# Optimization experiments

Measured on AMD Instinct MI355X. Metric: run time of the kernel, lower is better.

## Reference

```python
import jax, jax.numpy as jnp
import numpy as np

HIDDEN = 4096
NUM_HEADS = 32
HEAD_DIM = 128
NUM_KV_HEADS = 8
KV_GROUPS = NUM_HEADS // NUM_KV_HEADS
ROPE_THETA = 10000.0
SEQ = 2048
BATCH = 1
NEG_INF = -1e9


def fake_quant_int8(x):
    """Per-tensor symmetric int8 fake quantization (absmax scale)."""
    scale = jnp.maximum(jnp.max(jnp.abs(x)) / 127.0, 1e-8)
    q = jnp.clip(jnp.round(x / scale), -127.0, 127.0) * scale
    # straight-through estimator (no-op in fwd-only, keeps code shared)
    return x + jax.lax.stop_gradient(q - x)


def rotate_half(x):
    x1, x2 = jnp.split(x, 2, axis=-1)
    return jnp.concatenate([-x2, x1], axis=-1)


def rope_cos_sin(position_ids):
    inv_freq = 1.0 / (ROPE_THETA ** (jnp.arange(0, HEAD_DIM, 2, dtype=jnp.float32) / HEAD_DIM))
    freqs = position_ids.astype(jnp.float32)[..., None] * inv_freq  # [B,S,HD/2]
    emb = jnp.concatenate([freqs, freqs], axis=-1)                  # [B,S,HD]
    return jnp.cos(emb), jnp.sin(emb)


def setup_inputs() -> dict:
    key = jax.random.key(0)
    k1, k2, k3, k4, k5 = jax.random.split(key, 5)
    hidden_states = jax.random.normal(k1, (BATCH, SEQ, HIDDEN), dtype=jnp.float32)
    causal = jnp.tril(jnp.ones((SEQ, SEQ), dtype=bool))
    attention_mask = jnp.where(causal, 0.0, NEG_INF).astype(jnp.float32)[None, None]  # [1,1,S,S]
    position_ids = jnp.arange(SEQ, dtype=jnp.int64 if jax.config.jax_enable_x64 else jnp.int32)[None, :]
    s = 0.02
    wq = jax.random.normal(k2, (NUM_HEADS * HEAD_DIM, HIDDEN), dtype=jnp.float32) * s
    wk = jax.random.normal(k3, (NUM_KV_HEADS * HEAD_DIM, HIDDEN), dtype=jnp.float32) * s
    wv = jax.random.normal(k4, (NUM_KV_HEADS * HEAD_DIM, HIDDEN), dtype=jnp.float32) * s
    wo = jax.random.normal(k5, (HIDDEN, NUM_HEADS * HEAD_DIM), dtype=jnp.float32) * s
    return {"hidden_states": hidden_states, "attention_mask": attention_mask,
            "position_ids": position_ids, "wq": wq, "wk": wk, "wv": wv, "wo": wo}


def reference(hidden_states, attention_mask, position_ids, wq, wk, wv, wo):
    B, S, _ = hidden_states.shape

    def qlinear(x, w):  # quantized linear: fake-quant act and weight, y = x @ w.T
        return fake_quant_int8(x) @ fake_quant_int8(w).T

    q = qlinear(hidden_states, wq).reshape(B, S, NUM_HEADS, HEAD_DIM).transpose(0, 2, 1, 3)
    k = qlinear(hidden_states, wk).reshape(B, S, NUM_KV_HEADS, HEAD_DIM).transpose(0, 2, 1, 3)
    v = qlinear(hidden_states, wv).reshape(B, S, NUM_KV_HEADS, HEAD_DIM).transpose(0, 2, 1, 3)

    cos, sin = rope_cos_sin(position_ids)      # [B,S,HD]
    cos, sin = cos[:, None], sin[:, None]      # [B,1,S,HD]
    q = q * cos + rotate_half(q) * sin
    k = k * cos + rotate_half(k) * sin

    # repeat_kv: GQA -> full heads
    k = jnp.repeat(k, KV_GROUPS, axis=1)
    v = jnp.repeat(v, KV_GROUPS, axis=1)

    # quantized QK^T
    scores = jnp.einsum('bhqd,bhkd->bhqk', fake_quant_int8(q), fake_quant_int8(k))
    scores = scores * (1.0 / np.sqrt(HEAD_DIM).astype(np.float32))
    scores = scores + attention_mask[:, :, :, :S]
    probs = jax.nn.softmax(scores.astype(jnp.float32), axis=-1).astype(q.dtype)
    # attention_dropout = 0.0 -> identity

    # quantized AV
    attn_out = jnp.einsum('bhqk,bhkd->bhqd', fake_quant_int8(probs), fake_quant_int8(v))
    attn_out = attn_out.transpose(0, 2, 1, 3).reshape(B, S, NUM_HEADS * HEAD_DIM)
    return qlinear(attn_out, wo)
```

## Files before the change

kernel.cpp:

```cpp
#include <hip/hip_runtime.h>
#include <stdint.h>

#define SEQ   2048
#define HID   4096
#define NH    32
#define NKV   8
#define KVDIM 1024
#define KVCAT 2048

typedef int v4i __attribute__((ext_vector_type(4)));

#define VMCNT0 asm volatile("s_waitcnt vmcnt(0)" ::: "memory")

__device__ __forceinline__ void gload16(const void* g, void* l) {
    __builtin_amdgcn_global_load_lds(
        (const __attribute__((address_space(1))) void*)(uintptr_t)g,
        (__attribute__((address_space(3))) void*)(uintptr_t)l, 16, 0, 0);
}

__device__ __forceinline__ float slot_scale(const unsigned* slots, int slot) {
    return fmaxf(__uint_as_float(slots[slot << 5]) / 127.0f, 1e-8f);
}

__device__ __forceinline__ int q8v(float x, float s) {
    int v = (int)rintf(x / s);
    return v < -127 ? -127 : (v > 127 ? 127 : v);
}

__device__ __forceinline__ float fexp2(float x) {
    float r; asm("v_exp_f32 %0, %1" : "=v"(r) : "v"(x)); return r;
}

__device__ __forceinline__ float amax4(const float* __restrict__ p, long v) {
    float4 x = *(const float4*)(p + v * 4);
    return fmaxf(fmaxf(fabsf(x.x), fabsf(x.y)), fmaxf(fabsf(x.z), fabsf(x.w)));
}

__device__ __forceinline__ void block_amax_part(float m, float* dst) {
    __shared__ float sm[4];
    int lane = threadIdx.x & 63, w = threadIdx.x >> 6;
    for (int off = 32; off; off >>= 1) m = fmaxf(m, __shfl_xor(m, off, 64));
    if (lane == 0) sm[w] = m;
    __syncthreads();
    if (threadIdx.x == 0)
        *dst = fmaxf(fmaxf(sm[0], sm[1]), fmaxf(sm[2], sm[3]));
    __syncthreads();
}

#define NV0 ((long)SEQ * HID / 4)
#define NV1 ((long)HID * HID / 4)
#define NV2 ((long)KVDIM * HID / 4)
__global__ void k_absmax5(const float* __restrict__ a0, const float* __restrict__ a1,
                          const float* __restrict__ a2, const float* __restrict__ a3,
                          const float* __restrict__ a4, float* __restrict__ part) {
    int b = blockIdx.x;
    const float* p; long n; int lb, nb;
    if (b < 342)       { p = a0; n = NV0; lb = b;        nb = 342; }
    else if (b < 1025) { p = a1; n = NV1; lb = b - 342;  nb = 683; }
    else if (b < 1196) { p = a2; n = NV2; lb = b - 1025; nb = 171; }
    else if (b < 1367) { p = a3; n = NV2; lb = b - 1196; nb = 171; }
    else               { p = a4; n = NV1; lb = b - 1367; nb = 681; }
    long str = (long)nb * 256;
    float mm[8] = {0.f, 0.f, 0.f, 0.f, 0.f, 0.f, 0.f, 0.f};
    long v = (long)lb * 256 + threadIdx.x;
    for (; v + 7 * str < n; v += 8 * str) {
        #pragma unroll
        for (int j = 0; j < 8; j++) mm[j] = fmaxf(mm[j], amax4(p, v + j * str));
    }
    for (; v < n; v += str) mm[0] = fmaxf(mm[0], amax4(p, v));
    float m = fmaxf(fmaxf(fmaxf(mm[0], mm[1]), fmaxf(mm[2], mm[3])),
                    fmaxf(fmaxf(mm[4], mm[5]), fmaxf(mm[6], mm[7])));
    block_amax_part(m, part + blockIdx.x);
}

__global__ void k_reduceA(const float* __restrict__ part, unsigned* slots) {
    __shared__ float sm[4];
    const int lo[5] = {0, 342, 1025, 1196, 1367};
    const int hi[5] = {342, 1025, 1196, 1367, 2048};
    int t = threadIdx.x, lane = t & 63, w = t >> 6;
    for (int s = 0; s < 5; s++) {
        float m = 0.f;
        for (int i = lo[s] + t; i < hi[s]; i += 256) m = fmaxf(m, part[i]);
        for (int off = 32; off; off >>= 1) m = fmaxf(m, __shfl_xor(m, off, 64));
        if (lane == 0) sm[w] = m;
        __syncthreads();
        if (t == 0)
            slots[s << 5] = __float_as_uint(fmaxf(fmaxf(sm[0], sm[1]), fmaxf(sm[2], sm[3])));
        __syncthreads();
    }
}

__global__ void k_reduceB(const float* __restrict__ p1, const float* __restrict__ p2,
                          const float* __restrict__ p3, unsigned* slots) {
    __shared__ float sm[4];
    int t = threadIdx.x, lane = t & 63, w = t >> 6;
    const float* ps[3] = {p1, p2, p3};
    const int cnt[3] = {512, 128, 128};
    const int sl[3] = {5, 6, 7};
    for (int s = 0; s < 3; s++) {
        float m = 0.f;
        for (int i = t; i < cnt[s]; i += 256) m = fmaxf(m, ps[s][i]);
        for (int off = 32; off; off >>= 1) m = fmaxf(m, __shfl_xor(m, off, 64));
        if (lane == 0) sm[w] = m;
        __syncthreads();
        if (t == 0)
            slots[sl[s] << 5] = __float_as_uint(fmaxf(fmaxf(sm[0], sm[1]), fmaxf(sm[2], sm[3])));
        __syncthreads();
    }
}

__device__ __forceinline__ void qstore4(const float* __restrict__ src, long v,
                                        int8_t* __restrict__ dst, float s) {
    float4 x = *(const float4*)(src + v * 4);
    unsigned pa = (unsigned)(uint8_t)(int8_t)q8v(x.x, s)
                | ((unsigned)(uint8_t)(int8_t)q8v(x.y, s) << 8)
                | ((unsigned)(uint8_t)(int8_t)q8v(x.z, s) << 16)
                | ((unsigned)(uint8_t)(int8_t)q8v(x.w, s) << 24);
    *(unsigned*)(dst + v * 4) = pa;
}

__global__ void k_quant4(const float* __restrict__ a0, const float* __restrict__ a1,
                         const float* __restrict__ a2, const float* __restrict__ a3,
                         int8_t* __restrict__ d0, int8_t* __restrict__ d1,
                         int8_t* __restrict__ d2, int8_t* __restrict__ d3,
                         const unsigned* __restrict__ slots) {
    int b = blockIdx.x;
    const float* p; int8_t* d; long n; int slot, lb, nb;
    if (b < 512)       { p = a0; d = d0; n = NV0; slot = 0; lb = b;        nb = 512; }
    else if (b < 1536) { p = a1; d = d1; n = NV1; slot = 1; lb = b - 512;  nb = 1024; }
    else if (b < 1792) { p = a2; d = d2; n = NV2; slot = 2; lb = b - 1536; nb = 256; }
    else               { p = a3; d = d3; n = NV2; slot = 3; lb = b - 1792; nb = 256; }
    float s = slot_scale(slots, slot);
    long str = (long)nb * 256;
    long v = (long)lb * 256 + threadIdx.x;
    for (; v + 3 * str < n; v += 4 * str) {
        #pragma unroll
        for (int j = 0; j < 4; j++) qstore4(p, v + j * str, d, s);
    }
    for (; v < n; v += str) qstore4(p, v, d, s);
}

__global__ void k_quant(const float* __restrict__ x, int8_t* __restrict__ q, long nvec,
                        int rshift, long cmaskv, long ld,
                        const unsigned* __restrict__ slots, int slot) {
    float s = slot_scale(slots, slot);
    long gs = (long)gridDim.x * blockDim.x;
    long v = blockIdx.x * (long)blockDim.x + threadIdx.x;
    for (; v + 3 * gs < nvec; v += 4 * gs) {
        #pragma unroll
        for (int j = 0; j < 4; j++) {
            long vid = v + j * gs;
            long r = vid >> rshift;
            long c = (vid & cmaskv) << 2;
            float4 vv = *(const float4*)(x + r * ld + c);
            unsigned pa = (unsigned)(uint8_t)(int8_t)q8v(vv.x, s)
                        | ((unsigned)(uint8_t)(int8_t)q8v(vv.y, s) << 8)
                        | ((unsigned)(uint8_t)(int8_t)q8v(vv.z, s) << 16)
                        | ((unsigned)(uint8_t)(int8_t)q8v(vv.w, s) << 24);
            *(unsigned*)(q + vid * 4) = pa;
        }
    }
    for (; v < nvec; v += gs) {
        long r = v >> rshift;
        long c = (v & cmaskv) << 2;
        float4 vv = *(const float4*)(x + r * ld + c);
        unsigned pa = (unsigned)(uint8_t)(int8_t)q8v(vv.x, s)
                    | ((unsigned)(uint8_t)(int8_t)q8v(vv.y, s) << 8)
                    | ((unsigned)(uint8_t)(int8_t)q8v(vv.z, s) << 16)
                    | ((unsigned)(uint8_t)(int8_t)q8v(vv.w, s) << 24);
        *(unsigned*)(q + v * 4) = pa;
    }
}

__global__ void k_ropetab(const int* __restrict__ pos, float* __restrict__ ct,
                          float* __restrict__ st) {
    int tid = blockIdx.x * blockDim.x + threadIdx.x;
    if (tid >= SEQ * 64) return;
    int i = tid & 63, s = tid >> 6;
    double inv = 1.0 / pow(10000.0, (double)((float)(2 * i) * (1.0f / 128.0f)));
    float invf = (float)inv;
    float angf = (float)pos[s] * invf;
    double a = (double)angf;
    ct[tid] = (float)cos(a);
    st[tid] = (float)sin(a);
}

__global__ void k_transq(const float* __restrict__ src, long lds_, int8_t* __restrict__ dst,
                         long ldd, const unsigned* __restrict__ slots, int slot) {
    __shared__ float t[32][33];
    float s = slot_scale(slots, slot);
    int bx = blockIdx.x, by = blockIdx.y;
    int tid = threadIdx.x;
    int c = tid & 31, r0 = tid >> 5;
    #pragma unroll
    for (int j = 0; j < 4; j++) {
        int r = r0 + j * 8;
        t[r][c] = src[(long)(by * 32 + r) * lds_ + bx * 32 + c];
    }
    __syncthreads();
    int d = tid >> 3, k4 = (tid & 7) * 4;
    unsigned pa = 0;
    #pragma unroll
    for (int j = 0; j < 4; j++) {
        int iv = q8v(t[k4 + j][d], s);
        pa |= ((unsigned)(uint8_t)(int8_t)iv) << (8 * j);
    }
    *(unsigned*)(dst + (long)(bx * 32 + d) * ldd + by * 32 + k4) = pa;
}

__global__ __launch_bounds__(256) void k_gemm_i8(
    const int8_t* __restrict__ A, const int8_t* __restrict__ B, float* __restrict__ C,
    int M, int N, int K, unsigned* slots,
    int slotA, int slotB, int slotB2, int nsplit,
    float* pQ, float* pK, float* pV, int ropemode,
    const float* __restrict__ ct, const float* __restrict__ st) {
    __shared__ int8_t POOL[65536];
    int8_t (*As)[16384] = (int8_t(*)[16384])POOL;
    int8_t (*Bs)[16384] = (int8_t(*)[16384])(POOL + 32768);
    const v4i vzero = {0, 0, 0, 0};
    int tid = threadIdx.x, lane = tid & 63, wid = tid >> 6;
    int nbx = N >> 7;
    int nwg = gridDim.x, wg = blockIdx.x;
    int cpx = nwg >> 3;
    int swz = (wg & 7) * cpx + (wg >> 3);
    int bm = swz / nbx, bn = swz % nbx;
    long rowA0 = (long)bm * 128, colB0 = (long)bn * 128;
    int wrow = (wid >> 1) * 64, wcol = (wid & 1) * 64;
    int lr = lane >> 3;
    int swc = ((lane & 7) ^ lr) * 16;
    const int8_t* ga = A + (rowA0 + wid * 8 + lr) * (long)K + swc;
    const int8_t* gb = B + (colB0 + wid * 8 + lr) * (long)K + swc;
    v4i acc[4][4];
    #pragma unroll
    for (int m = 0; m < 4; m++)
        #pragma unroll
        for (int n = 0; n < 4; n++) acc[m][n] = vzero;

    auto STAGE = [&](int buf, int kt) {
        #pragma unroll
        for (int i = 0; i < 4; i++) {
            gload16(ga + kt + (long)(i * 32) * K, &As[buf][(wid * 8 + i * 32) * 128]);
            gload16(gb + kt + (long)(i * 32) * K, &Bs[buf][(wid * 8 + i * 32) * 128]);
        }
    };
    auto COMPUTE = [&](int buf) {
        #pragma unroll
        for (int ks = 0; ks < 2; ks++) {
            v4i af[4], bf[4];
            #pragma unroll
            for (int m = 0; m < 4; m++) {
                int row = wrow + m * 16 + (lane & 15);
                af[m] = *(const v4i*)(&As[buf][row * 128 + (((ks * 4 + (lane >> 4)) ^ (row & 7)) * 16)]);
            }
            #pragma unroll
            for (int n = 0; n < 4; n++) {
                int row = wcol + n * 16 + (lane & 15);
                bf[n] = *(const v4i*)(&Bs[buf][row * 128 + (((ks * 4 + (lane >> 4)) ^ (row & 7)) * 16)]);
            }
            #pragma unroll
            for (int m = 0; m < 4; m++)
                #pragma unroll
                for (int n = 0; n < 4; n++)
                    acc[m][n] = __builtin_amdgcn_mfma_i32_16x16x64_i8(af[m], bf[n], acc[m][n], 0, 0, 0);
        }
    };

    STAGE(0, 0);
    VMCNT0;
    __syncthreads();
    int nt = K >> 7, cur = 0;
    for (int t = 0; t < nt - 1; t++) {
        STAGE(cur ^ 1, (t + 1) << 7);
        COMPUTE(cur);
        VMCNT0;
        __syncthreads();
        cur ^= 1;
    }
    COMPUTE(cur);

    float sA = slot_scale(slots, slotA);
    float sB1 = slot_scale(slots, slotB);
    float sB2 = slot_scale(slots, slotB2);
    int qc = lane & 15, rgrp = (lane >> 4) << 2;
    if (ropemode == 1 || (ropemode == 2 && bn < 8)) {
        __syncthreads();
        float* EX = (float*)POOL;
        #pragma unroll
        for (int m = 0; m < 4; m++)
            #pragma unroll
            for (int n = 0; n < 4; n++) {
                int coll = wcol + n * 16 + qc;
                #pragma unroll
                for (int r = 0; r < 4; r++) {
                    int rowl = wrow + m * 16 + rgrp + r;
                    EX[rowl * 128 + (coll ^ ((rowl & 1) << 4))] = sA * sB1 * (float)acc[m][n][r];
                }
            }
        __syncthreads();
        float am = 0.f;
        #pragma unroll
        for (int m = 0; m < 4; m++)
            #pragma unroll
            for (int n = 0; n < 4; n++) {
                int coll = wcol + n * 16 + qc;
                #pragma unroll
                for (int r = 0; r < 4; r++) {
                    int rowl = wrow + m * 16 + rgrp + r;
                    long srow = rowA0 + rowl;
                    float self = EX[rowl * 128 + (coll ^ ((rowl & 1) << 4))];
                    float pv = EX[rowl * 128 + ((coll ^ 64) ^ ((rowl & 1) << 4))];
                    float c = ct[srow * 64 + (coll & 63)];
                    float sn = st[srow * 64 + (coll & 63)];
                    float o = (coll < 64) ? self * c - pv * sn : self * c + pv * sn;
                    am = fmaxf(am, fabsf(o));
                    C[srow * N + colB0 + coll] = o;
                }
            }
        block_amax_part(am, (ropemode == 1) ? pQ + blockIdx.x : pK + bm * 8 + (bn & 7));
    } else if (ropemode == 2) {
        float am = 0.f;
        #pragma unroll
        for (int m = 0; m < 4; m++) {
            long row0 = rowA0 + wrow + m * 16 + rgrp;
            #pragma unroll
            for (int n = 0; n < 4; n++) {
                int col = (int)colB0 + wcol + n * 16 + qc;
                float sc = sA * ((col < nsplit) ? sB1 : sB2);
                float* cp = C + row0 * N + col;
                #pragma unroll
                for (int r = 0; r < 4; r++) {
                    float val = sc * (float)acc[m][n][r];
                    cp[(long)r * N] = val;
                    am = fmaxf(am, fabsf(val));
                }
            }
        }
        block_amax_part(am, pV + bm * 8 + (bn & 7));
    } else {
        #pragma unroll
        for (int m = 0; m < 4; m++) {
            long row0 = rowA0 + wrow + m * 16 + rgrp;
            #pragma unroll
            for (int n = 0; n < 4; n++) {
                int col = (int)colB0 + wcol + n * 16 + qc;
                float sc = sA * ((col < nsplit) ? sB1 : sB2);
                float* cp = C + row0 * N + col;
                #pragma unroll
                for (int r = 0; r < 4; r++) cp[(long)r * N] = sc * (float)acc[m][n][r];
            }
        }
    }
}

__global__ __launch_bounds__(256) void k_attn(
    const int8_t* __restrict__ Qq, const int8_t* __restrict__ Kq, const int8_t* __restrict__ Vtq,
    int* __restrict__ AO, unsigned* slots) {
    __shared__ int8_t Qs[64 * 128];
    __shared__ int8_t Ks[2][64 * 128];
    __shared__ int8_t Vs[2][128 * 64];
    __shared__ int smx[4];
    const v4i vzero = {0, 0, 0, 0};
    const int NEGS = -(1 << 29);
    const float MAGIC = 12582912.0f;
    int tid = threadIdx.x, lane = tid & 63, w = tid >> 6;
    int qlan = lane & 15, g = lane >> 4;
    int idx = blockIdx.x;
    int qb = 31 - (idx >> 5), h = idx & 31, kvh = h >> 2;
    float sq = slot_scale(slots, 5), sk = slot_scale(slots, 6);
    float c2 = sq * sk * 0.08838834764831845f * 1.4426950408889634f;
    int lr8 = lane >> 3;
    int swc = ((lane & 7) ^ lr8) * 16;
    int lr4 = lane >> 2;
    int vswc = ((lane & 3) ^ (lr4 & 3)) * 16;
    const int8_t* kbase = Kq + ((long)(w * 8 + lr8)) * KVDIM + kvh * 128 + swc;
    const int8_t* vbase = Vtq + ((long)kvh * 128 + w * 16 + lr4) * SEQ + vswc;
    auto STAGE_K = [&](int buf, int kt) {
        #pragma unroll
        for (int i = 0; i < 2; i++)
            gload16(kbase + ((long)kt * 64 + i * 32) * KVDIM, &Ks[buf][(w * 8 + i * 32) * 128]);
    };
    auto STAGE_V = [&](int buf, int kt) {
        #pragma unroll
        for (int i = 0; i < 2; i++)
            gload16(vbase + (long)(i * 64) * SEQ + kt * 64, &Vs[buf][(w * 16 + i * 64) * 64]);
    };
    {
        const int8_t* qbase = Qq + ((long)qb * 64 + w * 8 + lr8) * HID + h * 128 + swc;
        #pragma unroll
        for (int i = 0; i < 2; i++)
            gload16(qbase + (long)(i * 32) * HID, &Qs[(w * 8 + i * 32) * 128]);
    }
    STAGE_K(0, 0);
    VMCNT0;
    __syncthreads();
    v4i aq[2];
    #pragma unroll
    for (int ks = 0; ks < 2; ks++) {
        int row = w * 16 + qlan;
        aq[ks] = *(const v4i*)(&Qs[row * 128 + (((ks * 4 + g) ^ (row & 7)) * 16)]);
    }
    int mi = -(1 << 30);
    float l = 0.f;
    int buf = 0;
    for (int kt = 0; kt <= qb; kt++) {
        if (kt < qb) STAGE_K(buf ^ 1, kt + 1);
        v4i sf[4] = {vzero, vzero, vzero, vzero};
        __builtin_amdgcn_s_setprio(1);
        #pragma unroll
        for (int ks = 0; ks < 2; ks++)
            #pragma unroll
            for (int f = 0; f < 4; f++) {
                int row = f * 16 + qlan;
                v4i bk = *(const v4i*)(&Ks[buf][row * 128 + (((ks * 4 + g) ^ (row & 7)) * 16)]);
                sf[f] = __builtin_amdgcn_mfma_i32_16x16x64_i8(bk, aq[ks], sf[f], 0, 0, 0);
            }
        __builtin_amdgcn_s_setprio(0);
        int sv[16];
        if (kt == qb) {
            int qthr = w * 16 + qlan;
            #pragma unroll
            for (int f = 0; f < 4; f++)
                #pragma unroll
                for (int r = 0; r < 4; r++) {
                    int kl = f * 16 + g * 4 + r;
                    sv[f * 4 + r] = (kl > qthr) ? NEGS : sf[f][r];
                }
        } else {
            #pragma unroll
            for (int f = 0; f < 4; f++)
                #pragma unroll
                for (int r = 0; r < 4; r++) sv[f * 4 + r] = sf[f][r];
        }
        int tm = sv[0];
        #pragma unroll
        for (int e = 1; e < 16; e++) tm = tm > sv[e] ? tm : sv[e];
        tm = max(tm, __shfl_xor(tm, 16, 64));
        tm = max(tm, __shfl_xor(tm, 32, 64));
        int mn = tm > mi ? tm : mi;
        float nb = -c2 * (float)mn;
        float esc = fexp2(fmaf((float)mi, c2, nb));
        float es = 0.f;
        #pragma unroll
        for (int e = 0; e < 16; e++) es += fexp2(fmaf((float)sv[e], c2, nb));
        es += __shfl_xor(es, 16, 64);
        es += __shfl_xor(es, 32, 64);
        l = l * esc + es;
        mi = mn;
        VMCNT0;
        __syncthreads();
        buf ^= 1;
    }
    float Bq = fmaf(c2, (float)mi, __log2f(l) - 6.9886846867721655f);
    unsigned* Ps32 = (unsigned*)Qs;
    int pwr = w * 320;
    v4i of[8];
    #pragma unroll
    for (int nf = 0; nf < 8; nf++) of[nf] = vzero;
    STAGE_K(0, 0);
    STAGE_V(0, 0);
    VMCNT0;
    __syncthreads();
    buf = 0;
    for (int kt = 0; kt <= qb; kt++) {
        if (kt < qb) { STAGE_K(buf ^ 1, kt + 1); STAGE_V(buf ^ 1, kt + 1); }
        v4i sf[4] = {vzero, vzero, vzero, vzero};
        __builtin_amdgcn_s_setprio(1);
        #pragma unroll
        for (int ks = 0; ks < 2; ks++)
            #pragma unroll
            for (int f = 0; f < 4; f++) {
                int row = f * 16 + qlan;
                v4i bk = *(const v4i*)(&Ks[buf][row * 128 + (((ks * 4 + g) ^ (row & 7)) * 16)]);
                sf[f] = __builtin_amdgcn_mfma_i32_16x16x64_i8(bk, aq[ks], sf[f], 0, 0, 0);
            }
        __builtin_amdgcn_s_setprio(0);
        if (kt == qb) {
            int qthr = w * 16 + qlan;
            #pragma unroll
            for (int f = 0; f < 4; f++) {
                unsigned pk = 0;
                #pragma unroll
                for (int r = 0; r < 4; r++) {
                    int kl = f * 16 + g * 4 + r;
                    int s = (kl > qthr) ? NEGS : sf[f][r];
                    float t = fexp2(fmaf((float)s, c2, -Bq));
                    unsigned u = __float_as_uint(t + MAGIC) & 127u;
                    pk |= u << (8 * r);
                }
                Ps32[pwr + (4 * f + g) * 20 + qlan] = pk;
            }
        } else {
            #pragma unroll
            for (int f = 0; f < 4; f++) {
                unsigned pk = 0;
                #pragma unroll
                for (int r = 0; r < 4; r++) {
                    float t = fexp2(fmaf((float)sf[f][r], c2, -Bq));
                    unsigned u = __float_as_uint(t + MAGIC) & 127u;
                    pk |= u << (8 * r);
                }
                Ps32[pwr + (4 * f + g) * 20 + qlan] = pk;
            }
        }
        int rb = pwr + 80 * g + qlan;
        v4i ap;
        ap[0] = (int)Ps32[rb];
        ap[1] = (int)Ps32[rb + 20];
        ap[2] = (int)Ps32[rb + 40];
        ap[3] = (int)Ps32[rb + 60];
        __builtin_amdgcn_s_setprio(1);
        #pragma unroll
        for (int nf = 0; nf < 8; nf++) {
            int row = nf * 16 + qlan;
            v4i bv = *(const v4i*)(&Vs[buf][row * 64 + ((g ^ (row & 3)) * 16)]);
            of[nf] = __builtin_amdgcn_mfma_i32_16x16x64_i8(ap, bv, of[nf], 0, 0, 0);
        }
        __builtin_amdgcn_s_setprio(0);
        VMCNT0;
        __syncthreads();
        buf ^= 1;
    }
    int mymax = 0;
    #pragma unroll
    for (int nf = 0; nf < 8; nf++)
        #pragma unroll
        for (int r = 0; r < 4; r++) {
            int val = of[nf][r];
            int av = val < 0 ? -val : val;
            mymax = av > mymax ? av : mymax;
            int qg = qb * 64 + w * 16 + 4 * g + r;
            AO[(long)qg * HID + h * 128 + nf * 16 + qlan] = val;
        }
    #pragma unroll
    for (int off = 1; off < 64; off <<= 1) {
        int o2 = __shfl_xor(mymax, off, 64);
        mymax = o2 > mymax ? o2 : mymax;
    }
    if (lane == 0) smx[w] = mymax;
    __syncthreads();
    if (tid == 0) {
        int mm = max(max(smx[0], smx[1]), max(smx[2], smx[3]));
        atomicMax(slots + (8 << 5), (unsigned)mm);
    }
}

__global__ void k_quant_ao(const int* __restrict__ a, int8_t* __restrict__ q, unsigned* slots) {
    float sv = slot_scale(slots, 7);
    float spv = (1.0f / 127.0f) * sv;
    float amax = spv * (float)(int)slots[8 << 5];
    float s = fmaxf(amax / 127.0f, 1e-8f);
    long nvec = (long)SEQ * HID / 4;
    long gs = (long)gridDim.x * blockDim.x;
    long v = blockIdx.x * (long)blockDim.x + threadIdx.x;
    for (; v + 3 * gs < nvec; v += 4 * gs) {
        #pragma unroll
        for (int j = 0; j < 4; j++) {
            long vid = v + j * gs;
            int4 x = *(const int4*)(a + vid * 4);
            int a0 = q8v(spv * (float)x.x, s);
            int a1 = q8v(spv * (float)x.y, s);
            int a2 = q8v(spv * (float)x.z, s);
            int a3 = q8v(spv * (float)x.w, s);
            unsigned pa = (unsigned)(uint8_t)(int8_t)a0
                        | ((unsigned)(uint8_t)(int8_t)a1 << 8)
                        | ((unsigned)(uint8_t)(int8_t)a2 << 16)
                        | ((unsigned)(uint8_t)(int8_t)a3 << 24);
            *(unsigned*)(q + vid * 4) = pa;
        }
    }
    for (; v < nvec; v += gs) {
        int4 x = *(const int4*)(a + v * 4);
        int a0 = q8v(spv * (float)x.x, s);
        int a1 = q8v(spv * (float)x.y, s);
        int a2 = q8v(spv * (float)x.z, s);
        int a3 = q8v(spv * (float)x.w, s);
        unsigned pa = (unsigned)(uint8_t)(int8_t)a0
                    | ((unsigned)(uint8_t)(int8_t)a1 << 8)
                    | ((unsigned)(uint8_t)(int8_t)a2 << 16)
                    | ((unsigned)(uint8_t)(int8_t)a3 << 24);
        *(unsigned*)(q + v * 4) = pa;
    }
    if (blockIdx.x == 0 && threadIdx.x == 0) slots[9 << 5] = __float_as_uint(amax);
}

extern "C" void kernel_launch(void* const* d_in, const int* in_sizes, int n_in,
                              void* d_out, int out_size, void* d_ws, size_t ws_size,
                              hipStream_t stream) {
    (void)in_sizes; (void)n_in; (void)out_size;
    const float* hid = (const float*)d_in[0];
    const int* pos = (const int*)d_in[2];
    const float* wqp = (const float*)d_in[3];
    const float* wkp = (const float*)d_in[4];
    const float* wvp = (const float*)d_in[5];
    const float* wop = (const float*)d_in[6];
    float* out = (float*)d_out;
    char* ws = (char*)d_ws;

    size_t o = 0;
    auto alloc = [&](size_t sz) { size_t r = o; o += (sz + 255) & ~(size_t)255; return r; };
    unsigned* slots = (unsigned*)(ws + alloc(2048));
    float* P0 = (float*)(ws + alloc(2048 * 4));
    float* P1 = (float*)(ws + alloc(512 * 4));
    float* P2 = (float*)(ws + alloc(128 * 4));
    float* P3 = (float*)(ws + alloc(128 * 4));
    int8_t* Xq   = (int8_t*)(ws + alloc((size_t)SEQ * HID));
    int8_t* Wqq  = (int8_t*)(ws + alloc((size_t)HID * HID));
    int8_t* Wkvq = (int8_t*)(ws + alloc((size_t)KVCAT * HID));
    float*  Qf   = (float*)(ws + alloc((size_t)SEQ * HID * 4));
    float*  KVf  = (float*)(ws + alloc((size_t)SEQ * KVCAT * 4));
    int8_t* Qq   = (int8_t*)(ws + alloc((size_t)SEQ * HID));
    int8_t* Kq   = (int8_t*)(ws + alloc((size_t)SEQ * KVDIM));
    int8_t* Vtq  = (int8_t*)(ws + alloc((size_t)KVDIM * SEQ));
    float*  ctab = (float*)(ws + alloc((size_t)SEQ * 64 * 4));
    float*  stab = (float*)(ws + alloc((size_t)SEQ * 64 * 4));
    if (ws_size < o) return;
    int8_t* Woq = Wqq;
    int*    AOint = (int*)Qf;
    int8_t* AOq = Xq;

    hipMemsetAsync(slots, 0, 2048, stream);
    k_ropetab<<<SEQ * 64 / 256, 256, 0, stream>>>(pos, ctab, stab);
    k_absmax5<<<2048, 256, 0, stream>>>(hid, wqp, wkp, wvp, wop, P0);
    k_reduceA<<<1, 256, 0, stream>>>(P0, slots);
    k_quant4<<<2048, 256, 0, stream>>>(hid, wqp, wkp, wvp,
                                       Xq, Wqq, Wkvq, Wkvq + (size_t)KVDIM * HID, slots);
    k_gemm_i8<<<512, 256, 0, stream>>>(Xq, Wqq, Qf, SEQ, HID, HID, slots,
                                       0, 1, 1, 1 << 30, P1, nullptr, nullptr, 1, ctab, stab);
    k_gemm_i8<<<256, 256, 0, stream>>>(Xq, Wkvq, KVf, SEQ, KVCAT, HID, slots,
                                       0, 2, 3, KVDIM, nullptr, P2, P3, 2, ctab, stab);
    const long CALL = 0x3FFFFFFFL;
    k_quant<<<2048, 256, 0, stream>>>(wop, Woq, (long)HID * HID / 4, 40, CALL, 0, slots, 4);
    k_reduceB<<<1, 256, 0, stream>>>(P1, P2, P3, slots);
    k_quant<<<2048, 256, 0, stream>>>(Qf, Qq, (long)SEQ * HID / 4, 40, CALL, 0, slots, 5);
    k_quant<<<512, 256, 0, stream>>>(KVf, Kq, (long)SEQ * KVDIM / 4, 8, 255, KVCAT, slots, 6);
    k_transq<<<dim3(32, 64), 256, 0, stream>>>(KVf + KVDIM, KVCAT, Vtq, SEQ, slots, 7);
    k_attn<<<1024, 256, 0, stream>>>(Qq, Kq, Vtq, AOint, slots);
    k_quant_ao<<<2048, 256, 0, stream>>>(AOint, AOq, slots);
    k_gemm_i8<<<512, 256, 0, stream>>>(AOq, Woq, out, SEQ, HID, HID, slots,
                                       9, 4, 4, 1 << 30, nullptr, nullptr, nullptr, 0,
                                       nullptr, nullptr);
}
```

Before: 301.0 us.

## Store Q/KV/attention intermediates in fp16 and widen quantization kernels to 16 elements

Intermediate Q, KV projection outputs and attention outputs are now written as fp16 instead of fp32/int32, halving the traffic for those buffers between kernels. The quantization kernels now process 16 elements per thread with wider loads and stores and use fewer blocks, and the absmax loop issues all loads before reducing. Attention now writes dequantized fp16 values directly. fp16 storage could change rounding right at quantization boundaries, which risks small mismatches against the fp32 reference.

```diff
diff --git a/kernel.cpp b/kernel.cpp
--- a/kernel.cpp
+++ b/kernel.cpp
@@ -1,4 +1,5 @@
 #include <hip/hip_runtime.h>
+#include <hip/hip_fp16.h>
 #include <stdint.h>
 
 #define SEQ   2048
@@ -27,12 +28,18 @@
     return v < -127 ? -127 : (v > 127 ? 127 : v);
 }
 
+__device__ __forceinline__ unsigned pk4(float a, float b, float c, float d, float s) {
+    return (unsigned)(uint8_t)(int8_t)q8v(a, s)
+         | ((unsigned)(uint8_t)(int8_t)q8v(b, s) << 8)
+         | ((unsigned)(uint8_t)(int8_t)q8v(c, s) << 16)
+         | ((unsigned)(uint8_t)(int8_t)q8v(d, s) << 24);
+}
+
 __device__ __forceinline__ float fexp2(float x) {
     float r; asm("v_exp_f32 %0, %1" : "=v"(r) : "v"(x)); return r;
 }
 
-__device__ __forceinline__ float amax4(const float* __restrict__ p, long v) {
-    float4 x = *(const float4*)(p + v * 4);
+__device__ __forceinline__ float fmax4a(float4 x) {
     return fmaxf(fmaxf(fabsf(x.x), fabsf(x.y)), fmaxf(fabsf(x.z), fabsf(x.w)));
 }
 
@@ -64,10 +71,13 @@
     float mm[8] = {0.f, 0.f, 0.f, 0.f, 0.f, 0.f, 0.f, 0.f};
     long v = (long)lb * 256 + threadIdx.x;
     for (; v + 7 * str < n; v += 8 * str) {
-        #pragma unroll
-        for (int j = 0; j < 8; j++) mm[j] = fmaxf(mm[j], amax4(p, v + j * str));
-    }
-    for (; v < n; v += str) mm[0] = fmaxf(mm[0], amax4(p, v));
+        float4 t[8];
+        #pragma unroll
+        for (int j = 0; j < 8; j++) t[j] = *(const float4*)(p + (v + j * str) * 4);
+        #pragma unroll
+        for (int j = 0; j < 8; j++) mm[j] = fmaxf(mm[j], fmax4a(t[j]));
+    }
+    for (; v < n; v += str) mm[0] = fmaxf(mm[0], fmax4a(*(const float4*)(p + v * 4)));
     float m = fmaxf(fmaxf(fmaxf(mm[0], mm[1]), fmaxf(mm[2], mm[3])),
                     fmaxf(fmaxf(mm[4], mm[5]), fmaxf(mm[6], mm[7])));
     block_amax_part(m, part + blockIdx.x);
@@ -109,16 +119,9 @@
     }
 }
 
-__device__ __forceinline__ void qstore4(const float* __restrict__ src, long v,
-                                        int8_t* __restrict__ dst, float s) {
-    float4 x = *(const float4*)(src + v * 4);
-    unsigned pa = (unsigned)(uint8_t)(int8_t)q8v(x.x, s)
-                | ((unsigned)(uint8_t)(int8_t)q8v(x.y, s) << 8)
-                | ((unsigned)(uint8_t)(int8_t)q8v(x.z, s) << 16)
-                | ((unsigned)(uint8_t)(int8_t)q8v(x.w, s) << 24);
-    *(unsigned*)(dst + v * 4) = pa;
-}
-
+#define NU0 ((long)SEQ * HID / 16)
+#define NU1 ((long)HID * HID / 16)
+#define NU2 ((long)KVDIM * HID / 16)
 __global__ void k_quant4(const float* __restrict__ a0, const float* __restrict__ a1,
                          const float* __restrict__ a2, const float* __restrict__ a3,
                          int8_t* __restrict__ d0, int8_t* __restrict__ d1,
@@ -126,49 +129,60 @@
                          const unsigned* __restrict__ slots) {
     int b = blockIdx.x;
     const float* p; int8_t* d; long n; int slot, lb, nb;
-    if (b < 512)       { p = a0; d = d0; n = NV0; slot = 0; lb = b;        nb = 512; }
-    else if (b < 1536) { p = a1; d = d1; n = NV1; slot = 1; lb = b - 512;  nb = 1024; }
-    else if (b < 1792) { p = a2; d = d2; n = NV2; slot = 2; lb = b - 1536; nb = 256; }
-    else               { p = a3; d = d3; n = NV2; slot = 3; lb = b - 1792; nb = 256; }
+    if (b < 512)       { p = a0; d = d0; n = NU0; slot = 0; lb = b;        nb = 512; }
+    else if (b < 1536) { p = a1; d = d1; n = NU1; slot = 1; lb = b - 512;  nb = 1024; }
+    else if (b < 1792) { p = a2; d = d2; n = NU2; slot = 2; lb = b - 1536; nb = 256; }
+    else               { p = a3; d = d3; n = NU2; slot = 3; lb = b - 1792; nb = 256; }
     float s = slot_scale(slots, slot);
     long str = (long)nb * 256;
-    long v = (long)lb * 256 + threadIdx.x;
-    for (; v + 3 * str < n; v += 4 * str) {
-        #pragma unroll
-        for (int j = 0; j < 4; j++) qstore4(p, v + j * str, d, s);
-    }
-    for (; v < n; v += str) qstore4(p, v, d, s);
-}
-
-__global__ void k_quant(const float* __restrict__ x, int8_t* __restrict__ q, long nvec,
-                        int rshift, long cmaskv, long ld,
-                        const unsigned* __restrict__ slots, int slot) {
+    for (long u = (long)lb * 256 + threadIdx.x; u < n; u += str) {
+        const float4* src = (const float4*)(p + u * 16);
+        float4 t0 = src[0], t1 = src[1], t2 = src[2], t3 = src[3];
+        int4 o;
+        o.x = (int)pk4(t0.x, t0.y, t0.z, t0.w, s);
+        o.y = (int)pk4(t1.x, t1.y, t1.z, t1.w, s);
+        o.z = (int)pk4(t2.x, t2.y, t2.z, t2.w, s);
+        o.w = (int)pk4(t3.x, t3.y, t3.z, t3.w, s);
+        *(int4*)(d + u * 16) = o;
+    }
+}
+
+__global__ void k_quantw(const float* __restrict__ x, int8_t* __restrict__ q, long nu,
+                         const unsigned* __restrict__ slots, int slot) {
     float s = slot_scale(slots, slot);
     long gs = (long)gridDim.x * blockDim.x;
-    long v = blockIdx.x * (long)blockDim.x + threadIdx.x;
-    for (; v + 3 * gs < nvec; v += 4 * gs) {
-        #pragma unroll
-        for (int j = 0; j < 4; j++) {
-            long vid = v + j * gs;
-            long r = vid >> rshift;
-            long c = (vid & cmaskv) << 2;
-            float4 vv = *(const float4*)(x + r * ld + c);
-            unsigned pa = (unsigned)(uint8_t)(int8_t)q8v(vv.x, s)
-                        | ((unsigned)(uint8_t)(int8_t)q8v(vv.y, s) << 8)
-                        | ((unsigned)(uint8_t)(int8_t)q8v(vv.z, s) << 16)
-                        | ((unsigned)(uint8_t)(int8_t)q8v(vv.w, s) << 24);
-            *(unsigned*)(q + vid * 4) = pa;
-        }
-    }
-    for (; v < nvec; v += gs) {
-        long r = v >> rshift;
-        long c = (v & cmaskv) << 2;
-        float4 vv = *(const float4*)(x + r * ld + c);
-        unsigned pa = (unsigned)(uint8_t)(int8_t)q8v(vv.x, s)
-                    | ((unsigned)(uint8_t)(int8_t)q8v(vv.y, s) << 8)
-                    | ((unsigned)(uint8_t)(int8_t)q8v(vv.z, s) << 16)
-                    | ((unsigned)(uint8_t)(int8_t)q8v(vv.w, s) << 24);
-        *(unsigned*)(q + v * 4) = pa;
+    for (long u = blockIdx.x * (long)blockDim.x + threadIdx.x; u < nu; u += gs) {
+        const float4* src = (const float4*)(x + u * 16);
+        float4 t0 = src[0], t1 = src[1], t2 = src[2], t3 = src[3];
+        int4 o;
+        o.x = (int)pk4(t0.x, t0.y, t0.z, t0.w, s);
+        o.y = (int)pk4(t1.x, t1.y, t1.z, t1.w, s);
+        o.z = (int)pk4(t2.x, t2.y, t2.z, t2.w, s);
+        o.w = (int)pk4(t3.x, t3.y, t3.z, t3.w, s);
+        *(int4*)(q + u * 16) = o;
+    }
+}
+
+__device__ __forceinline__ unsigned pk4h(unsigned h2a, unsigned h2b, float s) {
+    __half2 a = *(__half2*)&h2a, b = *(__half2*)&h2b;
+    return pk4(__low2float(a), __high2float(a), __low2float(b), __high2float(b), s);
+}
+__global__ void k_quanth(const __half* __restrict__ x, int8_t* __restrict__ q, long nu,
+                         int rshift, long cmask, long ld,
+                         const unsigned* __restrict__ slots, int slot) {
+    float s = slot_scale(slots, slot);
+    long gs = (long)gridDim.x * blockDim.x;
+    for (long u = blockIdx.x * (long)blockDim.x + threadIdx.x; u < nu; u += gs) {
+        long row = u >> rshift;
+        long cu = u & cmask;
+        const int4* src = (const int4*)(x + row * ld + cu * 16);
+        int4 a = src[0], b = src[1];
+        int4 o;
+        o.x = (int)pk4h((unsigned)a.x, (unsigned)a.y, s);
+        o.y = (int)pk4h((unsigned)a.z, (unsigned)a.w, s);
+        o.z = (int)pk4h((unsigned)b.x, (unsigned)b.y, s);
+        o.w = (int)pk4h((unsigned)b.z, (unsigned)b.w, s);
+        *(int4*)(q + u * 16) = o;
     }
 }
 
@@ -185,7 +199,7 @@
     st[tid] = (float)sin(a);
 }
 
-__global__ void k_transq(const float* __restrict__ src, long lds_, int8_t* __restrict__ dst,
+__global__ void k_transq(const __half* __restrict__ src, long lds_, int8_t* __restrict__ dst,
                          long ldd, const unsigned* __restrict__ slots, int slot) {
     __shared__ float t[32][33];
     float s = slot_scale(slots, slot);
@@ -195,7 +209,7 @@
     #pragma unroll
     for (int j = 0; j < 4; j++) {
         int r = r0 + j * 8;
-        t[r][c] = src[(long)(by * 32 + r) * lds_ + bx * 32 + c];
+        t[r][c] = __half2float(src[(long)(by * 32 + r) * lds_ + bx * 32 + c]);
     }
     __syncthreads();
     int d = tid >> 3, k4 = (tid & 7) * 4;
@@ -209,7 +223,7 @@
 }
 
 __global__ __launch_bounds__(256) void k_gemm_i8(
-    const int8_t* __restrict__ A, const int8_t* __restrict__ B, float* __restrict__ C,
+    const int8_t* __restrict__ A, const int8_t* __restrict__ B, void* __restrict__ Cv,
     int M, int N, int K, unsigned* slots,
     int slotA, int slotB, int slotB2, int nsplit,
     float* pQ, float* pK, float* pV, int ropemode,
@@ -217,6 +231,8 @@
     __shared__ int8_t POOL[65536];
     int8_t (*As)[16384] = (int8_t(*)[16384])POOL;
     int8_t (*Bs)[16384] = (int8_t(*)[16384])(POOL + 32768);
+    float* Cf = (float*)Cv;
+    __half* Ch = (__half*)Cv;
     const v4i vzero = {0, 0, 0, 0};
     int tid = threadIdx.x, lane = tid & 63, wid = tid >> 6;
     int nbx = N >> 7;
@@ -313,7 +329,7 @@
                     float sn = st[srow * 64 + (coll & 63)];
                     float o = (coll < 64) ? self * c - pv * sn : self * c + pv * sn;
                     am = fmaxf(am, fabsf(o));
-                    C[srow * N + colB0 + coll] = o;
+                    Ch[srow * N + colB0 + coll] = __float2half(o);
                 }
             }
         block_amax_part(am, (ropemode == 1) ? pQ + blockIdx.x : pK + bm * 8 + (bn & 7));
@@ -326,11 +342,11 @@
             for (int n = 0; n < 4; n++) {
                 int col = (int)colB0 + wcol + n * 16 + qc;
                 float sc = sA * ((col < nsplit) ? sB1 : sB2);
-                float* cp = C + row0 * N + col;
+                __half* cp = Ch + row0 * N + col;
                 #pragma unroll
                 for (int r = 0; r < 4; r++) {
                     float val = sc * (float)acc[m][n][r];
-                    cp[(long)r * N] = val;
+                    cp[(long)r * N] = __float2half(val);
                     am = fmaxf(am, fabsf(val));
                 }
             }
@@ -344,7 +360,7 @@
             for (int n = 0; n < 4; n++) {
                 int col = (int)colB0 + wcol + n * 16 + qc;
                 float sc = sA * ((col < nsplit) ? sB1 : sB2);
-                float* cp = C + row0 * N + col;
+                float* cp = Cf + row0 * N + col;
                 #pragma unroll
                 for (int r = 0; r < 4; r++) cp[(long)r * N] = sc * (float)acc[m][n][r];
             }
@@ -354,7 +370,7 @@
 
 __global__ __launch_bounds__(256) void k_attn(
     const int8_t* __restrict__ Qq, const int8_t* __restrict__ Kq, const int8_t* __restrict__ Vtq,
-    int* __restrict__ AO, unsigned* slots) {
+    __half* __restrict__ AO, unsigned* slots) {
     __shared__ int8_t Qs[64 * 128];
     __shared__ int8_t Ks[2][64 * 128];
     __shared__ int8_t Vs[2][128 * 64];
@@ -367,6 +383,7 @@
     int idx = blockIdx.x;
     int qb = 31 - (idx >> 5), h = idx & 31, kvh = h >> 2;
     float sq = slot_scale(slots, 5), sk = slot_scale(slots, 6);
+    float spv = slot_scale(slots, 7) * (1.0f / 127.0f);
     float c2 = sq * sk * 0.08838834764831845f * 1.4426950408889634f;
     int lr8 = lane >> 3;
     int swc = ((lane & 7) ^ lr8) * 16;
@@ -529,7 +546,7 @@
             int av = val < 0 ? -val : val;
             mymax = av > mymax ? av : mymax;
             int qg = qb * 64 + w * 16 + 4 * g + r;
-            AO[(long)qg * HID + h * 128 + nf * 16 + qlan] = val;
+            AO[(long)qg * HID + h * 128 + nf * 16 + qlan] = __float2half(spv * (float)val);
         }
     #pragma unroll
     for (int off = 1; off < 64; off <<= 1) {
@@ -544,41 +561,23 @@
     }
 }
 
-__global__ void k_quant_ao(const int* __restrict__ a, int8_t* __restrict__ q, unsigned* slots) {
+__global__ void k_quant_ao(const __half* __restrict__ a, int8_t* __restrict__ q,
+                           unsigned* slots) {
     float sv = slot_scale(slots, 7);
     float spv = (1.0f / 127.0f) * sv;
     float amax = spv * (float)(int)slots[8 << 5];
     float s = fmaxf(amax / 127.0f, 1e-8f);
-    long nvec = (long)SEQ * HID / 4;
+    long nu = (long)SEQ * HID / 16;
     long gs = (long)gridDim.x * blockDim.x;
-    long v = blockIdx.x * (long)blockDim.x + threadIdx.x;
-    for (; v + 3 * gs < nvec; v += 4 * gs) {
-        #pragma unroll
-        for (int j = 0; j < 4; j++) {
-            long vid = v + j * gs;
-            int4 x = *(const int4*)(a + vid * 4);
-            int a0 = q8v(spv * (float)x.x, s);
-            int a1 = q8v(spv * (float)x.y, s);
-            int a2 = q8v(spv * (float)x.z, s);
-            int a3 = q8v(spv * (float)x.w, s);
-            unsigned pa = (unsigned)(uint8_t)(int8_t)a0
-                        | ((unsigned)(uint8_t)(int8_t)a1 << 8)
-                        | ((unsigned)(uint8_t)(int8_t)a2 << 16)
-                        | ((unsigned)(uint8_t)(int8_t)a3 << 24);
-            *(unsigned*)(q + vid * 4) = pa;
-        }
-    }
-    for (; v < nvec; v += gs) {
-        int4 x = *(const int4*)(a + v * 4);
-        int a0 = q8v(spv * (float)x.x, s);
-        int a1 = q8v(spv * (float)x.y, s);
-        int a2 = q8v(spv * (float)x.z, s);
-        int a3 = q8v(spv * (float)x.w, s);
-        unsigned pa = (unsigned)(uint8_t)(int8_t)a0
-                    | ((unsigned)(uint8_t)(int8_t)a1 << 8)
-                    | ((unsigned)(uint8_t)(int8_t)a2 << 16)
-                    | ((unsigned)(uint8_t)(int8_t)a3 << 24);
-        *(unsigned*)(q + v * 4) = pa;
+    for (long u = blockIdx.x * (long)blockDim.x + threadIdx.x; u < nu; u += gs) {
+        const int4* src = (const int4*)(a + u * 16);
+        int4 x = src[0], y = src[1];
+        int4 o;
+        o.x = (int)pk4h((unsigned)x.x, (unsigned)x.y, s);
+        o.y = (int)pk4h((unsigned)x.z, (unsigned)x.w, s);
+        o.z = (int)pk4h((unsigned)y.x, (unsigned)y.y, s);
+        o.w = (int)pk4h((unsigned)y.z, (unsigned)y.w, s);
+        *(int4*)(q + u * 16) = o;
     }
     if (blockIdx.x == 0 && threadIdx.x == 0) slots[9 << 5] = __float_as_uint(amax);
 }
@@ -606,8 +605,8 @@
     int8_t* Xq   = (int8_t*)(ws + alloc((size_t)SEQ * HID));
     int8_t* Wqq  = (int8_t*)(ws + alloc((size_t)HID * HID));
     int8_t* Wkvq = (int8_t*)(ws + alloc((size_t)KVCAT * HID));
-    float*  Qf   = (float*)(ws + alloc((size_t)SEQ * HID * 4));
-    float*  KVf  = (float*)(ws + alloc((size_t)SEQ * KVCAT * 4));
+    __half* Qf   = (__half*)(ws + alloc((size_t)SEQ * HID * 2));
+    __half* KVf  = (__half*)(ws + alloc((size_t)SEQ * KVCAT * 2));
     int8_t* Qq   = (int8_t*)(ws + alloc((size_t)SEQ * HID));
     int8_t* Kq   = (int8_t*)(ws + alloc((size_t)SEQ * KVDIM));
     int8_t* Vtq  = (int8_t*)(ws + alloc((size_t)KVDIM * SEQ));
@@ -615,7 +614,7 @@
     float*  stab = (float*)(ws + alloc((size_t)SEQ * 64 * 4));
     if (ws_size < o) return;
     int8_t* Woq = Wqq;
-    int*    AOint = (int*)Qf;
+    __half* AOh = Qf;
     int8_t* AOq = Xq;
 
     hipMemsetAsync(slots, 0, 2048, stream);
@@ -628,14 +627,14 @@
                                        0, 1, 1, 1 << 30, P1, nullptr, nullptr, 1, ctab, stab);
     k_gemm_i8<<<256, 256, 0, stream>>>(Xq, Wkvq, KVf, SEQ, KVCAT, HID, slots,
                                        0, 2, 3, KVDIM, nullptr, P2, P3, 2, ctab, stab);
+    k_quantw<<<1024, 256, 0, stream>>>(wop, Woq, (long)HID * HID / 16, slots, 4);
+    k_reduceB<<<1, 256, 0, stream>>>(P1, P2, P3, slots);
     const long CALL = 0x3FFFFFFFL;
-    k_quant<<<2048, 256, 0, stream>>>(wop, Woq, (long)HID * HID / 4, 40, CALL, 0, slots, 4);
-    k_reduceB<<<1, 256, 0, stream>>>(P1, P2, P3, slots);
-    k_quant<<<2048, 256, 0, stream>>>(Qf, Qq, (long)SEQ * HID / 4, 40, CALL, 0, slots, 5);
-    k_quant<<<512, 256, 0, stream>>>(KVf, Kq, (long)SEQ * KVDIM / 4, 8, 255, KVCAT, slots, 6);
+    k_quanth<<<1024, 256, 0, stream>>>(Qf, Qq, (long)SEQ * HID / 16, 40, CALL, 0, slots, 5);
+    k_quanth<<<512, 256, 0, stream>>>(KVf, Kq, (long)SEQ * KVDIM / 16, 6, 63, KVCAT, slots, 6);
     k_transq<<<dim3(32, 64), 256, 0, stream>>>(KVf + KVDIM, KVCAT, Vtq, SEQ, slots, 7);
-    k_attn<<<1024, 256, 0, stream>>>(Qq, Kq, Vtq, AOint, slots);
-    k_quant_ao<<<2048, 256, 0, stream>>>(AOint, AOq, slots);
+    k_attn<<<1024, 256, 0, stream>>>(Qq, Kq, Vtq, AOh, slots);
+    k_quant_ao<<<1024, 256, 0, stream>>>(AOh, AOq, slots);
     k_gemm_i8<<<512, 256, 0, stream>>>(AOq, Woq, out, SEQ, HID, HID, slots,
                                        9, 4, 4, 1 << 30, nullptr, nullptr, nullptr, 0,
                                        nullptr, nullptr);
```

After: 285.8 us. -5.0%, faster.
